# Performance work log

Hardware: AMD Instinct MI355X
Metric: run time of the kernel (lower is better)

## Reference

```python
import jax, jax.numpy as jnp
import numpy as np

ALPHA = 0.2  # LeakyReLU negative slope


def setup_inputs() -> dict:
    key = jax.random.key(0)
    ks = jax.random.split(key, 6)
    B, N, F_IN, F_OUT = 4, 4096, 128, 128
    return {
        "input": jax.random.normal(ks[0], (B, N, F_IN), dtype=jnp.float32),
        "adj": jax.random.uniform(ks[1], (B, N, N), dtype=jnp.float32),
        "W": jax.random.normal(ks[2], (F_IN, F_OUT), dtype=jnp.float32) * (np.sqrt(2.0) / np.sqrt(F_IN)),
        "a1": jax.random.normal(ks[3], (F_OUT, 1), dtype=jnp.float32) * 0.1,
        "a2": jax.random.normal(ks[4], (F_OUT, 1), dtype=jnp.float32) * 0.1,
        "bias": jax.random.normal(ks[5], (N, F_OUT), dtype=jnp.float32) * 0.02,
    }


def reference(input, adj, W, a1, a2, bias):
    # h = X @ W : [B, N, F_out]
    h = jnp.einsum("bnf,fo->bno", input, W)
    # additive attention scores: e[b,i,j] = leakyrelu(f1[b,i] + f2[b,j])
    f1 = h @ a1            # [B, N, 1]
    f2 = h @ a2            # [B, N, 1]
    e = f1 + jnp.swapaxes(f2, 1, 2)        # [B, N, N]
    e = jnp.where(e >= 0, e, ALPHA * e)    # LeakyReLU
    # NOTE: original multiplies adj into scores (not -inf masking) and
    # softmaxes over dim=1 (the first node axis), faithfully reproduced.
    attention = jax.nn.softmax(adj * e, axis=1)  # [B, N, N]
    # dropout p=0 / eval mode -> identity
    h_prime = jnp.einsum("bij,bjo->bio", attention, h) + bias[None, :, :]
    # in_features == out_features -> plain residual
    return h_prime + input
```

## Files before the change

### kernel.cpp

```cpp
#include <hip/hip_runtime.h>
#include <hip/hip_bf16.h>

typedef short short8 __attribute__((ext_vector_type(8)));
typedef float f32x4 __attribute__((ext_vector_type(4)));
typedef unsigned short u16;
typedef u16 u16x8 __attribute__((ext_vector_type(8)));

static constexpr float kAlpha = 0.2f;

static __device__ inline u16 f2bf(float f) {
  __hip_bfloat16 h = __float2bfloat16(f);
  return *reinterpret_cast<u16*>(&h);
}
static __device__ inline float bf2f(u16 v) {
  unsigned int u = ((unsigned int)v) << 16;
  return __uint_as_float(u);
}

__global__ __launch_bounds__(256) void k1_hW(const float* __restrict__ X,
                                             const float* __restrict__ W,
                                             u16* __restrict__ hbT) {
  int row0 = blockIdx.x * 8;
  int o = threadIdx.x & 127;
  int g = threadIdx.x >> 7;
  __shared__ float Xs[8][128];
#pragma unroll
  for (int s = 0; s < 4; ++s) {
    int idx = threadIdx.x + s * 256;
    Xs[idx >> 7][idx & 127] = X[(size_t)row0 * 128 + idx];
  }
  __syncthreads();
  float acc[4] = {0.f, 0.f, 0.f, 0.f};
  for (int k = 0; k < 128; ++k) {
    float w = W[k * 128 + o];
#pragma unroll
    for (int s = 0; s < 4; ++s) acc[s] += Xs[g + 2 * s][k] * w;
  }
  int b = row0 >> 12;
  int n0 = row0 & 4095;
#pragma unroll
  for (int s = 0; s < 4; ++s)
    hbT[((size_t)b * 128 + o) * 4096 + n0 + g + 2 * s] = f2bf(acc[s]);
}

__global__ __launch_bounds__(256) void k1b_f(const u16* __restrict__ hbT,
                                             const float* __restrict__ a1,
                                             const float* __restrict__ a2,
                                             float* __restrict__ f1,
                                             float* __restrict__ f2) {
  int idx = blockIdx.x * 256 + threadIdx.x;
  int b = idx >> 12;
  int n = idx & 4095;
  const u16* base = hbT + (size_t)b * 128 * 4096 + n;
  float s1 = 0.f, s2 = 0.f;
  for (int o = 0; o < 128; ++o) {
    float h = bf2f(base[(size_t)o * 4096]);
    s1 += h * a1[o];
    s2 += h * a2[o];
  }
  f1[idx] = s1;
  f2[idx] = s2;
}

__global__ __launch_bounds__(256) void k2_dpart(const float* __restrict__ adj,
                                                const float* __restrict__ f1,
                                                const float* __restrict__ f2,
                                                float* __restrict__ dpart) {
  int bid = blockIdx.x;
  int ic = bid & 31;
  int jt = (bid >> 5) & 15;
  int b = bid >> 9;
  int t = threadIdx.x;
  int c = t & 63, r = t >> 6;
  int j = jt * 256 + c * 4;
  const size_t badj = (size_t)b * 4096 * 4096;
  f32x4 f2v = *reinterpret_cast<const f32x4*>(&f2[b * 4096 + j]);
  const float* f1p = f1 + b * 4096;
  int row0 = ic * 128 + r;
  f32x4 sum = (f32x4){0.f, 0.f, 0.f, 0.f};
#pragma unroll 8
  for (int s = 0; s < 32; ++s) {
    int row = row0 + 4 * s;
    f32x4 a = *reinterpret_cast<const f32x4*>(&adj[badj + (size_t)row * 4096 + j]);
    float f1r = f1p[row];
#pragma unroll
    for (int k = 0; k < 4; ++k) {
      float e = f1r + f2v[k];
      e = e >= 0.f ? e : kAlpha * e;
      sum[k] += __expf(a[k] * e);
    }
  }
  __shared__ f32x4 red[256];
  red[t] = sum;
  __syncthreads();
  if (t < 64) {
    f32x4 tt = red[t] + red[t + 64] + red[t + 128] + red[t + 192];
    *reinterpret_cast<f32x4*>(&dpart[(size_t)(b * 32 + ic) * 4096 + j]) = tt;
  }
}

__global__ __launch_bounds__(256) void k2b_scale(const float* __restrict__ dpart,
                                                 const u16* __restrict__ hbT,
                                                 u16* __restrict__ hs) {
  int idx = blockIdx.x * 256 + threadIdx.x;
  int b = idx >> 12, j = idx & 4095;
  float s = 0.f;
#pragma unroll
  for (int ic = 0; ic < 32; ++ic) s += dpart[(size_t)(b * 32 + ic) * 4096 + j];
  float rd = 1.0f / s;
  const u16* src = hbT + (size_t)b * 128 * 4096 + j;
  u16* dst = hs + (size_t)b * 128 * 4096 + j;
#pragma unroll 4
  for (int o = 0; o < 128; ++o) {
    dst[(size_t)o * 4096] = f2bf(bf2f(src[(size_t)o * 4096]) * rd);
  }
}

#define LROW 72
__global__ __launch_bounds__(512) void k3_out(
    const float* __restrict__ adj, const u16* __restrict__ hs,
    const float* __restrict__ f1, const float* __restrict__ f2,
    const float* __restrict__ bias, const float* __restrict__ input,
    float* __restrict__ out) {
  int bid = blockIdx.x;
  int b = bid >> 6;
  int i0 = (bid & 63) * 64;
  int t = threadIdx.x;
  int lane = t & 63;
  int w = t >> 6;

  __shared__ u16 As[2][64 * LROW];
  __shared__ u16 Bs[2][128 * LROW];
  __shared__ float f2s[4096];

  const size_t badj = (size_t)b * 4096 * 4096;
  const u16* hb = hs + (size_t)b * 128 * 4096;

  {
    const f32x4* src = reinterpret_cast<const f32x4*>(f2 + b * 4096);
    f32x4* dst = reinterpret_cast<f32x4*>(f2s);
    dst[t] = src[t];
    dst[t + 512] = src[t + 512];
  }

  int rr = t >> 3;
  int c0 = (t & 7) * 8;
  int bo = t >> 2;
  int bc0 = (t & 3) * 16;

  float f1v = f1[b * 4096 + i0 + rr];

  f32x4 acc[4];
#pragma unroll
  for (int n = 0; n < 4; ++n) acc[n] = (f32x4){0.f, 0.f, 0.f, 0.f};

  int rg = w & 3;
  int ch = w >> 2;

  f32x4 raA0, raA1, raB0, raB1;
  u16x8 rbA0, rbA1, rbB0, rbB1;

#define PREFETCH(S, J0)                                                              \
  {                                                                                  \
    const f32x4* ap = reinterpret_cast<const f32x4*>(                                \
        adj + badj + (size_t)(i0 + rr) * 4096 + (J0) + c0);                          \
    ra##S##0 = ap[0];                                                                \
    ra##S##1 = ap[1];                                                                \
    const u16x8* bp =                                                                \
        reinterpret_cast<const u16x8*>(hb + (size_t)bo * 4096 + (J0) + bc0);         \
    rb##S##0 = bp[0];                                                                \
    rb##S##1 = bp[1];                                                                \
  }

#define STORE(S, J0, BUF)                                                            \
  {                                                                                  \
    f32x4 e0 = *reinterpret_cast<const f32x4*>(&f2s[(J0) + c0]);                     \
    f32x4 e1 = *reinterpret_cast<const f32x4*>(&f2s[(J0) + c0 + 4]);                 \
    u16x8 pv;                                                                        \
    _Pragma("unroll") for (int k = 0; k < 4; ++k) {                                  \
      float e = f1v + e0[k];                                                         \
      e = e >= 0.f ? e : kAlpha * e;                                                 \
      pv[k] = f2bf(__expf(ra##S##0[k] * e));                                         \
    }                                                                                \
    _Pragma("unroll") for (int k = 0; k < 4; ++k) {                                  \
      float e = f1v + e1[k];                                                         \
      e = e >= 0.f ? e : kAlpha * e;                                                 \
      pv[k + 4] = f2bf(__expf(ra##S##1[k] * e));                                     \
    }                                                                                \
    *reinterpret_cast<u16x8*>(&As[BUF][rr * LROW + c0]) = pv;                        \
    *reinterpret_cast<u16x8*>(&Bs[BUF][bo * LROW + bc0]) = rb##S##0;                 \
    *reinterpret_cast<u16x8*>(&Bs[BUF][bo * LROW + bc0 + 8]) = rb##S##1;             \
  }

#define DOMFMA(BUF)                                                                  \
  {                                                                                  \
    _Pragma("unroll") for (int kk = 0; kk < 64; kk += 32) {                          \
      short8 af = *reinterpret_cast<const short8*>(                                  \
          &As[BUF][(16 * rg + (lane & 15)) * LROW + kk + (lane >> 4) * 8]);          \
      _Pragma("unroll") for (int n = 0; n < 4; ++n) {                                \
        short8 bf = *reinterpret_cast<const short8*>(                                \
            &Bs[BUF][(64 * ch + n * 16 + (lane & 15)) * LROW + kk +                  \
                     (lane >> 4) * 8]);                                              \
        acc[n] = __builtin_amdgcn_mfma_f32_16x16x32_bf16(af, bf, acc[n], 0, 0, 0);   \
      }                                                                              \
    }                                                                                \
  }

  PREFETCH(A, 0);
  __syncthreads();

  for (int j0 = 0; j0 < 4096; j0 += 128) {
    PREFETCH(B, j0 + 64);
    STORE(A, j0, 0);
    __syncthreads();
    DOMFMA(0);
    if (j0 + 128 < 4096) PREFETCH(A, j0 + 128);
    STORE(B, j0 + 64, 1);
    __syncthreads();
    DOMFMA(1);
  }

  int colbase = ch * 64 + (lane & 15);
  int rowbase = i0 + rg * 16 + (lane >> 4) * 4;
#pragma unroll
  for (int n = 0; n < 4; ++n) {
    int o = colbase + n * 16;
#pragma unroll
    for (int q = 0; q < 4; ++q) {
      int i = rowbase + q;
      size_t oidx = ((size_t)b * 4096 + i) * 128 + o;
      out[oidx] = acc[n][q] + bias[i * 128 + o] + input[oidx];
    }
  }
}

extern "C" void kernel_launch(void* const* d_in, const int* in_sizes, int n_in,
                              void* d_out, int out_size, void* d_ws, size_t ws_size,
                              hipStream_t stream) {
  const float* input = (const float*)d_in[0];
  const float* adj = (const float*)d_in[1];
  const float* W = (const float*)d_in[2];
  const float* a1 = (const float*)d_in[3];
  const float* a2 = (const float*)d_in[4];
  const float* bias = (const float*)d_in[5];
  float* out = (float*)d_out;

  char* ws = (char*)d_ws;
  u16* hbT = (u16*)(ws);
  float* f1 = (float*)(ws + 4194304);
  float* f2 = (float*)(ws + 4259840);
  float* dpart = (float*)(ws + 4325376);
  u16* hs = (u16*)(ws + 6422528);

  k1_hW<<<2048, 256, 0, stream>>>(input, W, hbT);
  k1b_f<<<64, 256, 0, stream>>>(hbT, a1, a2, f1, f2);
  k2_dpart<<<2048, 256, 0, stream>>>(adj, f1, f2, dpart);
  k2b_scale<<<64, 256, 0, stream>>>(dpart, hbT, hs);
  k3_out<<<256, 512, 0, stream>>>(adj, hs, f1, f2, bias, input, out);
}
```

Measured before the change: 152.0 us.

## Load MFMA operands directly from global memory, removing LDS staging and barriers

Each wave now loads its adj rows and h columns straight into registers in the MFMA fragment layout. It computes the exp scores in registers and feeds them to MFMA without going through shared memory or calling __syncthreads. This removes LDS traffic and barrier stalls and adds launch_bounds occupancy 2. In exchange, the two waves that share a row group (ch=0 and ch=1) each load the same adj row and recompute the same exp values, so adj reads and exp work are duplicated. The per-lane global loads are also less coalesced.

```diff
diff --git a/kernel.cpp b/kernel.cpp
--- a/kernel.cpp
+++ b/kernel.cpp
@@ -116,8 +116,7 @@
   }
 }
 
-#define LROW 72
-__global__ __launch_bounds__(512) void k3_out(
+__global__ __launch_bounds__(512, 2) void k3_out(
     const float* __restrict__ adj, const u16* __restrict__ hs,
     const float* __restrict__ f1, const float* __restrict__ f2,
     const float* __restrict__ bias, const float* __restrict__ input,
@@ -129,98 +128,113 @@
   int lane = t & 63;
   int w = t >> 6;
 
-  __shared__ u16 As[2][64 * LROW];
-  __shared__ u16 Bs[2][128 * LROW];
-  __shared__ float f2s[4096];
+  int rg = w & 3;
+  int ch = w >> 2;
 
   const size_t badj = (size_t)b * 4096 * 4096;
   const u16* hb = hs + (size_t)b * 128 * 4096;
 
-  {
-    const f32x4* src = reinterpret_cast<const f32x4*>(f2 + b * 4096);
-    f32x4* dst = reinterpret_cast<f32x4*>(f2s);
-    dst[t] = src[t];
-    dst[t + 512] = src[t + 512];
-  }
-
-  int rr = t >> 3;
-  int c0 = (t & 7) * 8;
-  int bo = t >> 2;
-  int bc0 = (t & 3) * 16;
-
-  float f1v = f1[b * 4096 + i0 + rr];
+  int l15 = lane & 15;
+  int l8 = (lane >> 4) * 8;
+
+  const float* aptr = adj + badj + (size_t)(i0 + 16 * rg + l15) * 4096 + l8;
+  const float* fptr = f2 + b * 4096 + l8;
+  const u16* hp0 = hb + (size_t)(64 * ch + 0 * 16 + l15) * 4096 + l8;
+  const u16* hp1 = hb + (size_t)(64 * ch + 1 * 16 + l15) * 4096 + l8;
+  const u16* hp2 = hb + (size_t)(64 * ch + 2 * 16 + l15) * 4096 + l8;
+  const u16* hp3 = hb + (size_t)(64 * ch + 3 * 16 + l15) * 4096 + l8;
+
+  float f1v = f1[b * 4096 + i0 + 16 * rg + l15];
 
   f32x4 acc[4];
 #pragma unroll
   for (int n = 0; n < 4; ++n) acc[n] = (f32x4){0.f, 0.f, 0.f, 0.f};
 
-  int rg = w & 3;
-  int ch = w >> 2;
-
-  f32x4 raA0, raA1, raB0, raB1;
-  u16x8 rbA0, rbA1, rbB0, rbB1;
-
-#define PREFETCH(S, J0)                                                              \
-  {                                                                                  \
-    const f32x4* ap = reinterpret_cast<const f32x4*>(                                \
-        adj + badj + (size_t)(i0 + rr) * 4096 + (J0) + c0);                          \
-    ra##S##0 = ap[0];                                                                \
-    ra##S##1 = ap[1];                                                                \
-    const u16x8* bp =                                                                \
-        reinterpret_cast<const u16x8*>(hb + (size_t)bo * 4096 + (J0) + bc0);         \
-    rb##S##0 = bp[0];                                                                \
-    rb##S##1 = bp[1];                                                                \
-  }
-
-#define STORE(S, J0, BUF)                                                            \
-  {                                                                                  \
-    f32x4 e0 = *reinterpret_cast<const f32x4*>(&f2s[(J0) + c0]);                     \
-    f32x4 e1 = *reinterpret_cast<const f32x4*>(&f2s[(J0) + c0 + 4]);                 \
-    u16x8 pv;                                                                        \
-    _Pragma("unroll") for (int k = 0; k < 4; ++k) {                                  \
-      float e = f1v + e0[k];                                                         \
-      e = e >= 0.f ? e : kAlpha * e;                                                 \
-      pv[k] = f2bf(__expf(ra##S##0[k] * e));                                         \
-    }                                                                                \
-    _Pragma("unroll") for (int k = 0; k < 4; ++k) {                                  \
-      float e = f1v + e1[k];                                                         \
-      e = e >= 0.f ? e : kAlpha * e;                                                 \
-      pv[k + 4] = f2bf(__expf(ra##S##1[k] * e));                                     \
-    }                                                                                \
-    *reinterpret_cast<u16x8*>(&As[BUF][rr * LROW + c0]) = pv;                        \
-    *reinterpret_cast<u16x8*>(&Bs[BUF][bo * LROW + bc0]) = rb##S##0;                 \
-    *reinterpret_cast<u16x8*>(&Bs[BUF][bo * LROW + bc0 + 8]) = rb##S##1;             \
-  }
-
-#define DOMFMA(BUF)                                                                  \
-  {                                                                                  \
-    _Pragma("unroll") for (int kk = 0; kk < 64; kk += 32) {                          \
-      short8 af = *reinterpret_cast<const short8*>(                                  \
-          &As[BUF][(16 * rg + (lane & 15)) * LROW + kk + (lane >> 4) * 8]);          \
-      _Pragma("unroll") for (int n = 0; n < 4; ++n) {                                \
-        short8 bf = *reinterpret_cast<const short8*>(                                \
-            &Bs[BUF][(64 * ch + n * 16 + (lane & 15)) * LROW + kk +                  \
-                     (lane >> 4) * 8]);                                              \
-        acc[n] = __builtin_amdgcn_mfma_f32_16x16x32_bf16(af, bf, acc[n], 0, 0, 0);   \
-      }                                                                              \
-    }                                                                                \
-  }
-
-  PREFETCH(A, 0);
-  __syncthreads();
-
+  f32x4 raA0, raA1, raA2, raA3, raB0, raB1, raB2, raB3;
+  u16x8 rbA0, rbA1, rbA2, rbA3, rbA4, rbA5, rbA6, rbA7;
+  u16x8 rbB0, rbB1, rbB2, rbB3, rbB4, rbB5, rbB6, rbB7;
+
+#define PF(S, J0)                                                  \
+  {                                                                \
+    int jj = (J0) & 4095;  \
+    ra##S##0 = *reinterpret_cast<const f32x4*>(aptr + jj);         \
+    ra##S##1 = *reinterpret_cast<const f32x4*>(aptr + jj + 4);     \
+    ra##S##2 = *reinterpret_cast<const f32x4*>(aptr + jj + 32);    \
+    ra##S##3 = *reinterpret_cast<const f32x4*>(aptr + jj + 36);    \
+    rb##S##0 = *reinterpret_cast<const u16x8*>(hp0 + jj);          \
+    rb##S##1 = *reinterpret_cast<const u16x8*>(hp1 + jj);          \
+    rb##S##2 = *reinterpret_cast<const u16x8*>(hp2 + jj);          \
+    rb##S##3 = *reinterpret_cast<const u16x8*>(hp3 + jj);          \
+    rb##S##4 = *reinterpret_cast<const u16x8*>(hp0 + jj + 32);     \
+    rb##S##5 = *reinterpret_cast<const u16x8*>(hp1 + jj + 32);     \
+    rb##S##6 = *reinterpret_cast<const u16x8*>(hp2 + jj + 32);     \
+    rb##S##7 = *reinterpret_cast<const u16x8*>(hp3 + jj + 32);     \
+  }
+
+#define COMPUTE(S, J0)                                                             \
+  {                                                                                \
+    int jj = (J0) & 4095;                                                          \
+    f32x4 g0 = *reinterpret_cast<const f32x4*>(fptr + jj);                         \
+    f32x4 g1 = *reinterpret_cast<const f32x4*>(fptr + jj + 4);                     \
+    f32x4 g2 = *reinterpret_cast<const f32x4*>(fptr + jj + 32);                    \
+    f32x4 g3 = *reinterpret_cast<const f32x4*>(fptr + jj + 36);                    \
+    u16x8 af;                                                                      \
+    _Pragma("unroll") for (int k = 0; k < 4; ++k) {                                \
+      float e = f1v + g0[k];                                                       \
+      e = e >= 0.f ? e : kAlpha * e;                                               \
+      af[k] = f2bf(__expf(ra##S##0[k] * e));                                       \
+    }                                                                              \
+    _Pragma("unroll") for (int k = 0; k < 4; ++k) {                                \
+      float e = f1v + g1[k];                                                       \
+      e = e >= 0.f ? e : kAlpha * e;                                               \
+      af[4 + k] = f2bf(__expf(ra##S##1[k] * e));                                   \
+    }                                                                              \
+    acc[0] = __builtin_amdgcn_mfma_f32_16x16x32_bf16(                              \
+        *reinterpret_cast<short8*>(&af), *reinterpret_cast<short8*>(&rb##S##0),    \
+        acc[0], 0, 0, 0);                                                          \
+    acc[1] = __builtin_amdgcn_mfma_f32_16x16x32_bf16(                              \
+        *reinterpret_cast<short8*>(&af), *reinterpret_cast<short8*>(&rb##S##1),    \
+        acc[1], 0, 0, 0);                                                          \
+    acc[2] = __builtin_amdgcn_mfma_f32_16x16x32_bf16(                              \
+        *reinterpret_cast<short8*>(&af), *reinterpret_cast<short8*>(&rb##S##2),    \
+        acc[2], 0, 0, 0);                                                          \
+    acc[3] = __builtin_amdgcn_mfma_f32_16x16x32_bf16(                              \
+        *reinterpret_cast<short8*>(&af), *reinterpret_cast<short8*>(&rb##S##3),    \
+        acc[3], 0, 0, 0);                                                          \
+    _Pragma("unroll") for (int k = 0; k < 4; ++k) {                                \
+      float e = f1v + g2[k];                                                       \
+      e = e >= 0.f ? e : kAlpha * e;                                               \
+      af[k] = f2bf(__expf(ra##S##2[k] * e));                                       \
+    }                                                                              \
+    _Pragma("unroll") for (int k = 0; k < 4; ++k) {                                \
+      float e = f1v + g3[k];                                                       \
+      e = e >= 0.f ? e : kAlpha * e;                                               \
+      af[4 + k] = f2bf(__expf(ra##S##3[k] * e));                                   \
+    }                                                                              \
+    acc[0] = __builtin_amdgcn_mfma_f32_16x16x32_bf16(                              \
+        *reinterpret_cast<short8*>(&af), *reinterpret_cast<short8*>(&rb##S##4),    \
+        acc[0], 0, 0, 0);                                                          \
+    acc[1] = __builtin_amdgcn_mfma_f32_16x16x32_bf16(                              \
+        *reinterpret_cast<short8*>(&af), *reinterpret_cast<short8*>(&rb##S##5),    \
+        acc[1], 0, 0, 0);                                                          \
+    acc[2] = __builtin_amdgcn_mfma_f32_16x16x32_bf16(                              \
+        *reinterpret_cast<short8*>(&af), *reinterpret_cast<short8*>(&rb##S##6),    \
+        acc[2], 0, 0, 0);                                                          \
+    acc[3] = __builtin_amdgcn_mfma_f32_16x16x32_bf16(                              \
+        *reinterpret_cast<short8*>(&af), *reinterpret_cast<short8*>(&rb##S##7),    \
+        acc[3], 0, 0, 0);                                                          \
+  }
+
+  PF(A, 0);
+  PF(B, 64);
   for (int j0 = 0; j0 < 4096; j0 += 128) {
-    PREFETCH(B, j0 + 64);
-    STORE(A, j0, 0);
-    __syncthreads();
-    DOMFMA(0);
-    if (j0 + 128 < 4096) PREFETCH(A, j0 + 128);
-    STORE(B, j0 + 64, 1);
-    __syncthreads();
-    DOMFMA(1);
-  }
-
-  int colbase = ch * 64 + (lane & 15);
+    COMPUTE(A, j0);
+    PF(A, j0 + 128);
+    COMPUTE(B, j0 + 64);
+    PF(B, j0 + 192);
+  }
+
+  int colbase = ch * 64 + l15;
   int rowbase = i0 + rg * 16 + (lane >> 4) * 4;
 #pragma unroll
   for (int n = 0; n < 4; ++n) {
```

Result: slower. 289.9 us (+90.7%).
